# Performance work log

Hardware: AMD Instinct MI355X
Metric: run time of the kernel (lower is better)

Reference implementation:

```python
import jax, jax.numpy as jnp
import numpy as np
import math

ETA = 1.0          # self.ddim_sampling_eta
SCALE = 1.0        # self.scale (unused in eval ddim path here)
IOU_THR = 0.5
SCORE_THR = 0.5


def cosine_alphas_cumprod(timesteps=1000, s=0.008):
    steps = timesteps + 1
    x = np.linspace(0, timesteps, steps, dtype=np.float64)
    ac = np.cos((x / timesteps + s) / (1 + s) * math.pi * 0.5) ** 2
    ac = ac / ac[0]
    betas = np.clip(1 - ac[1:] / ac[:-1], 0, 0.999)
    alphas = 1.0 - betas
    return np.cumprod(alphas).astype(np.float32)  # [timesteps]


def setup_inputs() -> dict:
    key = jax.random.key(0)
    ks = jax.random.split(key, 8)
    B, N, C, H = 128, 500, 80, 6
    boxes_t = jax.random.normal(ks[0], (B, N, 2), dtype=jnp.float32)
    predicted_class = jax.random.normal(ks[1], (H, B, N, C), dtype=jnp.float32)
    predicted_boxes = jax.random.uniform(ks[2], (H, B, N, 2), dtype=jnp.float32)
    noise = jax.random.normal(ks[3], (B, N, 2), dtype=jnp.float32)
    fresh_noise = jax.random.normal(ks[4], (B, N, 2), dtype=jnp.float32)
    alphas_cumprod = jnp.asarray(cosine_alphas_cumprod(1000))
    return {
        "boxes_t": boxes_t,
        "predicted_class": predicted_class,
        "predicted_boxes": predicted_boxes,
        "noise": noise,
        "fresh_noise": fresh_noise,
        "alphas_cumprod": alphas_cumprod,
        "t_now": 999,
        "t_next": 499,
    }


def _nms_1d_single(boxes_cw, scores, labels):
    # boxes_cw: [N,2] (center, width) 1-D intervals; class-aware greedy NMS.
    N = boxes_cw.shape[0]
    c = boxes_cw[:, 0]
    w = jnp.maximum(boxes_cw[:, 1], 1e-4)
    x1, x2 = c - w / 2, c + w / 2
    inter = jnp.maximum(0.0, jnp.minimum(x2[:, None], x2[None, :])
                        - jnp.maximum(x1[:, None], x1[None, :]))
    union = w[:, None] + w[None, :] - inter
    iou = inter / jnp.maximum(union, 1e-9)                       # [N,N]
    same = labels[:, None] == labels[None, :]
    order = jnp.argsort(-scores)
    iou_s = iou[order][:, order]
    same_s = same[order][:, order]
    idx = jnp.arange(N)

    def body(i, suppressed):
        keep_i = jnp.logical_not(suppressed[i])
        row = keep_i & (iou_s[i] > IOU_THR) & same_s[i] & (idx > i)
        return suppressed | row

    suppressed = jax.lax.fori_loop(0, N, body, jnp.zeros((N,), bool))
    keep_sorted = jnp.logical_not(suppressed)
    return jnp.zeros((N,), bool).at[order].set(keep_sorted)      # original order


def reference(boxes_t, predicted_class, predicted_boxes, noise, fresh_noise,
              alphas_cumprod, t_now, t_next):
    ac = alphas_cumprod
    boxes_start = predicted_boxes[-1]                            # [B,N,2]

    # predict_noise_from_start (extract -> scalar gather at t_now)
    sqrt_recip = jnp.sqrt(1.0 / ac[t_now])
    sqrt_recipm1 = jnp.sqrt(1.0 / ac[t_now] - 1.0)
    pred_noise = (sqrt_recip * boxes_t - boxes_start) / sqrt_recipm1

    # box renewal: keep mask from sigmoid-max of predicted_class[-1][0]
    score0 = jax.nn.sigmoid(predicted_class[-1][0])              # [N,C]
    keep = jnp.max(score0, axis=-1) > SCORE_THR                  # [N]

    # DDIM step
    alpha, alpha_next = ac[t_now], ac[t_next]
    sigma = ETA * jnp.sqrt((1 - alpha / alpha_next) * (1 - alpha_next) / (1 - alpha))
    cc = jnp.sqrt(1 - alpha_next - sigma ** 2)
    upd = boxes_start * jnp.sqrt(alpha_next) + cc * pred_noise + sigma * noise
    # removed slots are renewed with fresh gaussian proposals (mask form of concat)
    boxes_next = jnp.where(keep[None, :, None], upd, fresh_noise)  # [B,N,2]

    # postprocessing: softmax over classes (drop last bg class), max -> scores/labels
    probs = jax.nn.softmax(predicted_class[-1], axis=-1)[:, :, :-1]  # [B,N,C-1]
    scores = jnp.max(probs, axis=-1)                             # [B,N]
    labels = jnp.argmax(probs, axis=-1)                          # [B,N]
    nms_keep = jax.vmap(_nms_1d_single)(boxes_start, scores, labels)  # [B,N] bool

    return boxes_next, scores, labels, nms_keep
```

## Files before the change

### kernel.cpp

```cpp
#include <hip/hip_runtime.h>
#include <float.h>

#define BB 128
#define NN 500
#define CC 80
#define NH 6
#define NP 512
#define MS 9

typedef unsigned long long u64;
typedef unsigned int u32;

__global__ __launch_bounds__(256) void scores_labels_keep_kernel(
    const float* __restrict__ pc,
    float* __restrict__ scores,
    float* __restrict__ labels,
    int* __restrict__ keep) {
    const int rl = threadIdx.x >> 2;
    const int q = threadIdx.x & 3;
    const int row = blockIdx.x * 64 + rl;
    if (row >= BB * NN) return;

    const float4* base = (const float4*)(pc + (size_t)(NH - 1) * BB * NN * CC);
    float4 v[5];
#pragma unroll
    for (int k = 0; k < 5; ++k) v[k] = base[(size_t)row * 20 + q + 4 * k];

    float m = v[0].x;
#pragma unroll
    for (int k = 0; k < 5; ++k) {
        m = fmaxf(m, v[k].x); m = fmaxf(m, v[k].y);
        m = fmaxf(m, v[k].z); m = fmaxf(m, v[k].w);
    }
    m = fmaxf(m, __shfl_xor(m, 1));
    m = fmaxf(m, __shfl_xor(m, 2));

    float s = 0.0f;
#pragma unroll
    for (int k = 0; k < 5; ++k) {
        s += expf(v[k].x - m); s += expf(v[k].y - m);
        s += expf(v[k].z - m); s += expf(v[k].w - m);
    }
    s += __shfl_xor(s, 1);
    s += __shfl_xor(s, 2);

    float bv = -FLT_MAX; int bc = 1000;
#pragma unroll
    for (int k = 0; k < 5; ++k) {
        const float* vf = (const float*)&v[k];
#pragma unroll
        for (int j = 0; j < 4; ++j) {
            int c = (q + 4 * k) * 4 + j;
            float val = vf[j];
            if (c < CC - 1 && (val > bv || (val == bv && c < bc))) { bv = val; bc = c; }
        }
    }
#pragma unroll
    for (int off = 1; off < 4; off <<= 1) {
        float ov = __shfl_xor(bv, off);
        int oc = __shfl_xor(bc, off);
        if (ov > bv || (ov == bv && oc < bc)) { bv = ov; bc = oc; }
    }

    if (q == 0) {
        scores[row] = expf(bv - m) / s;
        labels[row] = (float)bc;
        if (row < NN) keep[row] = (m > 0.0f) ? 1 : 0;
    }
}

__global__ void boxes_next_kernel(const float* __restrict__ boxes_t,
                                  const float* __restrict__ pb,
                                  const float* __restrict__ noise,
                                  const float* __restrict__ fresh,
                                  const float* __restrict__ ac,
                                  const int* __restrict__ t_now_p,
                                  const int* __restrict__ t_next_p,
                                  const int* __restrict__ keep,
                                  float* __restrict__ out) {
    int i = blockIdx.x * blockDim.x + threadIdx.x;
    if (i >= BB * NN) return;
    int n = i % NN;
    int tn = t_now_p[0], tx = t_next_p[0];
    float a = ac[tn], an = ac[tx];
    float sqrt_recip = sqrtf(1.0f / a);
    float sqrt_recipm1 = sqrtf(1.0f / a - 1.0f);
    float sigma = sqrtf((1.0f - a / an) * (1.0f - an) / (1.0f - a));
    float cc = sqrtf(1.0f - an - sigma * sigma);
    float sqan = sqrtf(an);
    const float2 bt = ((const float2*)boxes_t)[i];
    const float2 bs = ((const float2*)(pb + (size_t)(NH - 1) * BB * NN * 2))[i];
    float2 o;
    if (keep[n]) {
        const float2 nz = ((const float2*)noise)[i];
        float pn0 = (sqrt_recip * bt.x - bs.x) / sqrt_recipm1;
        float pn1 = (sqrt_recip * bt.y - bs.y) / sqrt_recipm1;
        o.x = bs.x * sqan + cc * pn0 + sigma * nz.x;
        o.y = bs.y * sqan + cc * pn1 + sigma * nz.y;
    } else {
        o = ((const float2*)fresh)[i];
    }
    ((float2*)out)[i] = o;
}

__global__ __launch_bounds__(1024) void nms_kernel(const float* __restrict__ pb,
                                                   const float* __restrict__ scores,
                                                   const float* __restrict__ labels,
                                                   float* __restrict__ keep_out) {
    __shared__ float4 scs4[NP / 4];
    __shared__ float4 box4u[NP];
    __shared__ float4 sbox4[NP];
    __shared__ int order[NP];
    __shared__ u64 masks[NN * MS + 16];
    __shared__ u32 rem_lo[8], rem_hi[8];

    const int b = blockIdx.x;
    const int tid = threadIdx.x;
    float* scs = (float*)scs4;

    const float2* boxes = (const float2*)(pb + (size_t)(NH - 1) * BB * NN * 2) + (size_t)b * NN;
    const float* sc = scores + (size_t)b * NN;
    const float* lb = labels + (size_t)b * NN;

    if (tid < NP) {
        if (tid < NN) {
            float2 cw = boxes[tid];
            float w = fmaxf(cw.y, 0.0001f);
            box4u[tid] = make_float4(cw.x - w * 0.5f, cw.x + w * 0.5f, w,
                                     __int_as_float((int)lb[tid]));
            scs[tid] = sc[tid];
        } else {
            box4u[tid] = make_float4(0.f, 0.f, 0.f, __int_as_float(-1));
            scs[tid] = -FLT_MAX;
        }
    }
    __syncthreads();

    if (tid < NP) {
        float si = scs[tid];
        int r = 0;
        for (int j4 = 0; j4 < NP / 4; ++j4) {
            float4 s4 = scs4[j4];
            int j = j4 * 4;
            r += (s4.x > si) || (s4.x == si && (j + 0) < tid);
            r += (s4.y > si) || (s4.y == si && (j + 1) < tid);
            r += (s4.z > si) || (s4.z == si && (j + 2) < tid);
            r += (s4.w > si) || (s4.w == si && (j + 3) < tid);
        }
        order[r] = tid;
    }
    __syncthreads();

    if (tid < NP) sbox4[tid] = box4u[order[tid]];
    __syncthreads();

    {
        for (int t = tid; t < NN * 8; t += 1024) {
            int a = t >> 3, wd = t & 7;
            if (wd < (a >> 6)) masks[a * MS + wd] = 0ull;
        }
        const int wid = tid >> 6;
        const int lane = tid & 63;
        for (int p = wid; p < 64; p += 16) {
            const int ablk = p >> 3, wd = p & 7;
            if (wd < ablk) continue;
            const int a = ablk * 64 + lane;
            float4 me = (a < NN) ? sbox4[a] : make_float4(0.f, 0.f, 0.f, __int_as_float(-2));
            const int lk = __float_as_int(me.w);
            u64 m = 0ull;
            const int j1 = min(NN, wd * 64 + 64);
            for (int j = wd * 64; j < j1; ++j) {
                float4 ob = sbox4[j];
                float inter = fminf(me.y, ob.y) - fmaxf(me.x, ob.x);
                bool pre = (j > a) && (__float_as_int(ob.w) == lk) && (inter > 0.0f);
                if (pre) {
                    float uni = me.z + ob.z - inter;
                    float iou = inter / fmaxf(uni, 1e-9f);
                    if (iou > 0.5f) m |= 1ull << (j & 63);
                }
            }
            if (a < NN) masks[a * MS + wd] = m;
        }
    }
    __syncthreads();

    if (tid < 64) {
        const int lane = tid;
        const int lw = lane & 7;
        u32 lo = 0, hi = 0;
        u64 nextm = masks[0 * MS + lw];
        for (int i = 0; i < NN; ++i) {
            u64 mw = nextm;
            nextm = masks[(i + 1) * MS + lw];
            u32 colo = __builtin_amdgcn_readlane(lo, i >> 6);
            u32 cohi = __builtin_amdgcn_readlane(hi, i >> 6);
            u32 bit = (i & 32) ? ((cohi >> (i & 31)) & 1u) : ((colo >> (i & 31)) & 1u);
            u32 sel = bit ? 0u : 0xFFFFFFFFu;
            lo |= (u32)mw & sel;
            hi |= (u32)(mw >> 32) & sel;
        }
        if (lane < 8) { rem_lo[lane] = lo; rem_hi[lane] = hi; }
    }
    __syncthreads();

    if (tid < NN) {
        u32 word = (tid & 32) ? rem_hi[tid >> 6] : rem_lo[tid >> 6];
        u32 bit = (word >> (tid & 31)) & 1u;
        keep_out[(size_t)b * NN + order[tid]] = bit ? 0.0f : 1.0f;
    }
}

extern "C" void kernel_launch(void* const* d_in, const int* in_sizes, int n_in,
                              void* d_out, int out_size, void* d_ws, size_t ws_size,
                              hipStream_t stream) {
    const float* boxes_t = (const float*)d_in[0];
    const float* pc      = (const float*)d_in[1];
    const float* pb      = (const float*)d_in[2];
    const float* noise   = (const float*)d_in[3];
    const float* fresh   = (const float*)d_in[4];
    const float* ac      = (const float*)d_in[5];
    const int*   t_now   = (const int*)d_in[6];
    const int*   t_next  = (const int*)d_in[7];

    float* out_boxes  = (float*)d_out;
    float* out_scores = out_boxes + (size_t)BB * NN * 2;
    float* out_labels = out_scores + (size_t)BB * NN;
    float* out_keep   = out_labels + (size_t)BB * NN;

    int* keep_ws = (int*)d_ws;

    scores_labels_keep_kernel<<<(BB * NN) / 64, 256, 0, stream>>>(
        pc, out_scores, out_labels, keep_ws);
    boxes_next_kernel<<<(BB * NN + 255) / 256, 256, 0, stream>>>(
        boxes_t, pb, noise, fresh, ac, t_now, t_next, keep_ws, out_boxes);
    nms_kernel<<<BB, 1024, 0, stream>>>(pb, out_scores, out_labels, out_keep);
}
```

Measured before the change: 236.0 us.

## Replace bitmask NMS with per-class bucketed greedy suppression

The NMS kernel no longer builds a full 500x500 IoU bitmask followed by a serial 500-step sweep. It now counting-sorts the score-ordered boxes by label and runs greedy suppression independently per class, with one thread per class. The block shrinks from 1024 to 512 threads. This removes the quadratic mask build and the long single-wave serial loop, but each class is handled by one serial thread doing O(n^2) work, so load imbalance across classes can dominate.

```diff
diff --git a/kernel.cpp b/kernel.cpp
--- a/kernel.cpp
+++ b/kernel.cpp
@@ -6,7 +6,6 @@
 #define CC 80
 #define NH 6
 #define NP 512
-#define MS 9
 
 typedef unsigned long long u64;
 typedef unsigned int u32;
@@ -103,16 +102,20 @@
     ((float2*)out)[i] = o;
 }
 
-__global__ __launch_bounds__(1024) void nms_kernel(const float* __restrict__ pb,
-                                                   const float* __restrict__ scores,
-                                                   const float* __restrict__ labels,
-                                                   float* __restrict__ keep_out) {
+__global__ __launch_bounds__(512) void nms_kernel(const float* __restrict__ pb,
+                                                  const float* __restrict__ scores,
+                                                  const float* __restrict__ labels,
+                                                  float* __restrict__ keep_out) {
     __shared__ float4 scs4[NP / 4];
     __shared__ float4 box4u[NP];
     __shared__ float4 sbox4[NP];
     __shared__ int order[NP];
-    __shared__ u64 masks[NN * MS + 16];
-    __shared__ u32 rem_lo[8], rem_hi[8];
+    __shared__ unsigned char lab8[NP];
+    __shared__ short brank_s[NP];
+    __shared__ short member[NP];
+    __shared__ int hist[CC];
+    __shared__ int boff[CC];
+    __shared__ unsigned char supp[NP];
 
     const int b = blockIdx.x;
     const int tid = threadIdx.x;
@@ -122,21 +125,21 @@
     const float* sc = scores + (size_t)b * NN;
     const float* lb = labels + (size_t)b * NN;
 
-    if (tid < NP) {
-        if (tid < NN) {
-            float2 cw = boxes[tid];
-            float w = fmaxf(cw.y, 0.0001f);
-            box4u[tid] = make_float4(cw.x - w * 0.5f, cw.x + w * 0.5f, w,
-                                     __int_as_float((int)lb[tid]));
-            scs[tid] = sc[tid];
-        } else {
-            box4u[tid] = make_float4(0.f, 0.f, 0.f, __int_as_float(-1));
-            scs[tid] = -FLT_MAX;
-        }
-    }
-    __syncthreads();
-
-    if (tid < NP) {
+    if (tid < CC) hist[tid] = 0;
+    if (tid < NN) {
+        float2 cw = boxes[tid];
+        float w = fmaxf(cw.y, 0.0001f);
+        box4u[tid] = make_float4(cw.x - w * 0.5f, cw.x + w * 0.5f, w,
+                                 __int_as_float((int)lb[tid]));
+        scs[tid] = sc[tid];
+    } else {
+        box4u[tid] = make_float4(0.f, 0.f, 0.f, __int_as_float(255));
+        scs[tid] = -FLT_MAX;
+    }
+    supp[tid] = 0;
+    __syncthreads();
+
+    {
         float si = scs[tid];
         int r = 0;
         for (int j4 = 0; j4 < NP / 4; ++j4) {
@@ -151,62 +154,69 @@
     }
     __syncthreads();
 
-    if (tid < NP) sbox4[tid] = box4u[order[tid]];
-    __syncthreads();
-
     {
-        for (int t = tid; t < NN * 8; t += 1024) {
-            int a = t >> 3, wd = t & 7;
-            if (wd < (a >> 6)) masks[a * MS + wd] = 0ull;
-        }
-        const int wid = tid >> 6;
+        float4 v = box4u[order[tid]];
+        sbox4[tid] = v;
+        lab8[tid] = (unsigned char)__float_as_int(v.w);
+    }
+    __syncthreads();
+
+    if (tid < NN) {
+        const u32 myl = lab8[tid];
+        int cnt = 0;
+        const uint4* l16 = (const uint4*)lab8;
+        const int nc = (tid >> 4) + 1;
+        for (int cI = 0; cI < nc; ++cI) {
+            uint4 c = l16[cI];
+            int base = cI * 16;
+#pragma unroll
+            for (int byi = 0; byi < 4; ++byi) {
+                cnt += (base + byi      < tid) && (((c.x >> (8 * byi)) & 0xFF) == myl);
+                cnt += (base + 4 + byi  < tid) && (((c.y >> (8 * byi)) & 0xFF) == myl);
+                cnt += (base + 8 + byi  < tid) && (((c.z >> (8 * byi)) & 0xFF) == myl);
+                cnt += (base + 12 + byi < tid) && (((c.w >> (8 * byi)) & 0xFF) == myl);
+            }
+        }
+        brank_s[tid] = (short)cnt;
+        atomicAdd(&hist[myl], 1);
+    }
+    __syncthreads();
+    if (tid == 0) {
+        int s = 0;
+        for (int l = 0; l < CC; ++l) { boff[l] = s; s += hist[l]; }
+    }
+    __syncthreads();
+    if (tid < NN) member[boff[lab8[tid]] + brank_s[tid]] = (short)tid;
+    __syncthreads();
+
+    {
         const int lane = tid & 63;
-        for (int p = wid; p < 64; p += 16) {
-            const int ablk = p >> 3, wd = p & 7;
-            if (wd < ablk) continue;
-            const int a = ablk * 64 + lane;
-            float4 me = (a < NN) ? sbox4[a] : make_float4(0.f, 0.f, 0.f, __int_as_float(-2));
-            const int lk = __float_as_int(me.w);
-            u64 m = 0ull;
-            const int j1 = min(NN, wd * 64 + 64);
-            for (int j = wd * 64; j < j1; ++j) {
-                float4 ob = sbox4[j];
-                float inter = fminf(me.y, ob.y) - fmaxf(me.x, ob.x);
-                bool pre = (j > a) && (__float_as_int(ob.w) == lk) && (inter > 0.0f);
-                if (pre) {
-                    float uni = me.z + ob.z - inter;
-                    float iou = inter / fmaxf(uni, 1e-9f);
-                    if (iou > 0.5f) m |= 1ull << (j & 63);
+        const int wv = tid >> 6;
+        const int l = lane * 8 + wv;
+        if (l < CC) {
+            const int n = hist[l], off = boff[l];
+            for (int p = 0; p < n - 1; ++p) {
+                const int rp = member[off + p];
+                if (supp[rp]) continue;
+                const float4 bp = sbox4[rp];
+                for (int q = p + 1; q < n; ++q) {
+                    const int rq = member[off + q];
+                    if (supp[rq]) continue;
+                    const float4 bq = sbox4[rq];
+                    float inter = fminf(bp.y, bq.y) - fmaxf(bp.x, bq.x);
+                    if (inter > 0.0f) {
+                        float uni = bp.z + bq.z - inter;
+                        float iou = inter / fmaxf(uni, 1e-9f);
+                        if (iou > 0.5f) supp[rq] = 1;
+                    }
                 }
             }
-            if (a < NN) masks[a * MS + wd] = m;
-        }
-    }
-    __syncthreads();
-
-    if (tid < 64) {
-        const int lane = tid;
-        const int lw = lane & 7;
-        u32 lo = 0, hi = 0;
-        u64 nextm = masks[0 * MS + lw];
-        for (int i = 0; i < NN; ++i) {
-            u64 mw = nextm;
-            nextm = masks[(i + 1) * MS + lw];
-            u32 colo = __builtin_amdgcn_readlane(lo, i >> 6);
-            u32 cohi = __builtin_amdgcn_readlane(hi, i >> 6);
-            u32 bit = (i & 32) ? ((cohi >> (i & 31)) & 1u) : ((colo >> (i & 31)) & 1u);
-            u32 sel = bit ? 0u : 0xFFFFFFFFu;
-            lo |= (u32)mw & sel;
-            hi |= (u32)(mw >> 32) & sel;
-        }
-        if (lane < 8) { rem_lo[lane] = lo; rem_hi[lane] = hi; }
+        }
     }
     __syncthreads();
 
     if (tid < NN) {
-        u32 word = (tid & 32) ? rem_hi[tid >> 6] : rem_lo[tid >> 6];
-        u32 bit = (word >> (tid & 31)) & 1u;
-        keep_out[(size_t)b * NN + order[tid]] = bit ? 0.0f : 1.0f;
+        keep_out[(size_t)b * NN + order[tid]] = supp[tid] ? 0.0f : 1.0f;
     }
 }
 
@@ -233,5 +243,5 @@
         pc, out_scores, out_labels, keep_ws);
     boxes_next_kernel<<<(BB * NN + 255) / 256, 256, 0, stream>>>(
         boxes_t, pb, noise, fresh, ac, t_now, t_next, keep_ws, out_boxes);
-    nms_kernel<<<BB, 1024, 0, stream>>>(pb, out_scores, out_labels, out_keep);
-}
+    nms_kernel<<<BB, 512, 0, stream>>>(pb, out_scores, out_labels, out_keep);
+}
```

Result: faster. 221.9 us (-6.0%).
